# Optimization experiments

Measured on AMD Instinct MI355X. Metric: run time of the kernel, lower is better.

Reference implementation:

```python
import jax, jax.numpy as jnp
import numpy as np

N, E, D = 100000, 640000, 128  # nodes, edges, feature dim (in_dim == out_dim == 128)
BN_EPS = 1e-5


def setup_inputs() -> dict:
    key = jax.random.key(0)
    ks = jax.random.split(key, 8)
    x = jax.random.normal(ks[0], (N, D), dtype=jnp.float32)
    edge_index = jax.random.randint(ks[1], (2, E), 0, N, dtype=jnp.int64)
    s = 1.0 / np.sqrt(D)
    W1 = jax.random.uniform(ks[2], (D, D), jnp.float32, -s, s)
    b1 = jax.random.uniform(ks[3], (D,), jnp.float32, -s, s)
    W2 = jax.random.uniform(ks[4], (D, D), jnp.float32, -s, s)
    b2 = jax.random.uniform(ks[5], (D,), jnp.float32, -s, s)
    return {
        "x": x,
        "edge_index": edge_index,
        "eps": jnp.array([0.1], dtype=jnp.float32),
        "W1": W1, "b1": b1,
        "g1": jnp.ones((D,), jnp.float32), "beta1": jnp.zeros((D,), jnp.float32),
        "W2": W2, "b2": b2,
        "g2": jnp.ones((D,), jnp.float32), "beta2": jnp.zeros((D,), jnp.float32),
    }


def _batchnorm(h, gamma, beta):
    # BatchNorm1d in training mode: biased batch stats over the node dim
    mean = jnp.mean(h, axis=0)
    var = jnp.var(h, axis=0)
    return gamma * (h - mean) * jax.lax.rsqrt(var + BN_EPS) + beta


def reference(x, edge_index, eps, W1, b1, g1, beta1, W2, b2, g2, beta2):
    src, dst = edge_index[0], edge_index[1]
    # gather messages from source nodes, scatter-add into destination nodes
    aggr = jax.ops.segment_sum(x[src], dst, num_segments=x.shape[0])  # [N, D]
    h = (1.0 + eps) * x + aggr
    h = jax.nn.relu(_batchnorm(h @ W1.T + b1, g1, beta1))
    h = jax.nn.relu(_batchnorm(h @ W2.T + b2, g2, beta2))
    return h
```

## Files before the change

kernel.cpp:

```cpp
#include <hip/hip_runtime.h>

#define NN 100000
#define DD 128
#define EE 640000
#define NPAD 100352

typedef __bf16 bf16x8 __attribute__((ext_vector_type(8)));
typedef float floatx4 __attribute__((ext_vector_type(4)));

union BF8 {
    bf16x8 v;
    unsigned short u[8];
    int4 i4;
};

__device__ __forceinline__ unsigned short f2bf(float f) {
    unsigned int u = __float_as_uint(f);
    u += 0x7FFF + ((u >> 16) & 1);
    return (unsigned short)(u >> 16);
}

__global__ __launch_bounds__(256) void hist_k(const int* __restrict__ ei,
                                              int* __restrict__ deg) {
    int e = blockIdx.x * 256 + threadIdx.x;
    if (e < EE) atomicAdd(&deg[ei[EE + e]], 1);
}

__global__ __launch_bounds__(256) void scan1_k(const int* __restrict__ deg,
                                               int* __restrict__ exc,
                                               int* __restrict__ chunkSums) {
    __shared__ int s[256];
    int t = threadIdx.x, g = blockIdx.x * 256 + t;
    int v = (g < NN) ? deg[g] : 0;
    s[t] = v;
    __syncthreads();
    for (int off = 1; off < 256; off <<= 1) {
        int u = (t >= off) ? s[t - off] : 0;
        __syncthreads();
        s[t] += u;
        __syncthreads();
    }
    if (g < NN) exc[g] = s[t] - v;
    if (t == 255) chunkSums[blockIdx.x] = s[255];
}

__global__ __launch_bounds__(512) void scan2_k(int* __restrict__ chunkSums, int n) {
    __shared__ int s[512];
    int t = threadIdx.x;
    int v = (t < n) ? chunkSums[t] : 0;
    s[t] = v;
    __syncthreads();
    for (int off = 1; off < 512; off <<= 1) {
        int u = (t >= off) ? s[t - off] : 0;
        __syncthreads();
        s[t] += u;
        __syncthreads();
    }
    if (t < n) chunkSums[t] = s[t] - v;
}

__global__ __launch_bounds__(256) void scan3_k(int* __restrict__ exc,
                                               const int* __restrict__ chunkSums,
                                               int* __restrict__ cursor) {
    int g = blockIdx.x * 256 + threadIdx.x;
    if (g < NN) {
        int o = exc[g] + chunkSums[blockIdx.x];
        exc[g] = o;
        cursor[g] = o;
    }
}

__global__ __launch_bounds__(256) void esort_k(const int* __restrict__ ei,
                                               int* __restrict__ cursor,
                                               int* __restrict__ ssrc) {
    int e = blockIdx.x * 256 + threadIdx.x;
    if (e >= EE) return;
    int pos = atomicAdd(&cursor[ei[EE + e]], 1);
    ssrc[pos] = ei[e];
}

__global__ __launch_bounds__(256) void wconv_k(const float* __restrict__ W1,
                                               const float* __restrict__ W2,
                                               unsigned short* __restrict__ wb) {
    int i = blockIdx.x * 256 + threadIdx.x;
    const float4* s4 = (i < 4096) ? (const float4*)W1 : (const float4*)W2;
    float4 v = s4[i & 4095];
    ushort4 u;
    u.x = f2bf(v.x); u.y = f2bf(v.y); u.z = f2bf(v.z); u.w = f2bf(v.w);
    ((ushort4*)wb)[i] = u;
}

__global__ __launch_bounds__(256) void aggregate_k(
    const float4* __restrict__ x4, const int* __restrict__ ssrc,
    const int* __restrict__ offs, const int* __restrict__ deg,
    const float* __restrict__ epsp, ushort4* __restrict__ hout) {
    int tid = blockIdx.x * 256 + threadIdx.x;
    int node = tid >> 5, lane = tid & 31;
    if (node >= NN) return;
    int start = offs[node], d = deg[node];
    float ef = 1.0f + epsp[0];
    float4 v = x4[node * 32 + lane];
    float ax = ef * v.x, ay = ef * v.y, az = ef * v.z, aw = ef * v.w;
    for (int j = 0; j < d; j += 4) {
        int r = d - j;
        int b = start + j;
        int s0 = ssrc[b];
        int s1 = ssrc[b + ((r > 1) ? 1 : 0)];
        int s2 = ssrc[b + ((r > 2) ? 2 : 0)];
        int s3 = ssrc[b + ((r > 3) ? 3 : 0)];
        float4 xa = x4[s0 * 32 + lane];
        float4 xb = x4[s1 * 32 + lane];
        float4 xc = x4[s2 * 32 + lane];
        float4 xd = x4[s3 * 32 + lane];
        float m1 = (r > 1) ? 1.f : 0.f;
        float m2 = (r > 2) ? 1.f : 0.f;
        float m3 = (r > 3) ? 1.f : 0.f;
        ax += xa.x; ay += xa.y; az += xa.z; aw += xa.w;
        ax += m1 * xb.x; ay += m1 * xb.y; az += m1 * xb.z; aw += m1 * xb.w;
        ax += m2 * xc.x; ay += m2 * xc.y; az += m2 * xc.z; aw += m2 * xc.w;
        ax += m3 * xd.x; ay += m3 * xd.y; az += m3 * xd.z; aw += m3 * xd.w;
    }
    ushort4 u;
    u.x = f2bf(ax); u.y = f2bf(ay); u.z = f2bf(az); u.w = f2bf(aw);
    hout[node * 32 + lane] = u;
}

__global__ __launch_bounds__(256, 2) void gin_gemm_k(
    const unsigned short* __restrict__ hin,
    const unsigned short* __restrict__ Wbf, const float* __restrict__ bias,
    float* __restrict__ y, float* __restrict__ statsOut) {
    __shared__ __align__(16) float s_sum[128];
    __shared__ __align__(16) float s_sq[128];

    const int tid = threadIdx.x;
    const int l = tid & 63, w = tid >> 6;
    const int m = l & 15, q = l >> 4;

    if (tid < 128) { s_sum[tid] = 0.f; s_sq[tid] = 0.f; }

    bf16x8 wf[8][4];
#pragma unroll
    for (int ct = 0; ct < 8; ++ct) {
        const unsigned short* wr = Wbf + (size_t)(ct * 16 + m) * 128 + q * 8;
#pragma unroll
        for (int kc = 0; kc < 4; ++kc) {
            BF8 t;
            t.i4 = *(const int4*)(wr + kc * 32);
            wf[ct][kc] = t.v;
        }
    }
    float bc[8];
#pragma unroll
    for (int ct = 0; ct < 8; ++ct) bc[ct] = bias[ct * 16 + m];

    float ps[8], pq[8];
#pragma unroll
    for (int ct = 0; ct < 8; ++ct) { ps[ct] = 0.f; pq[ct] = 0.f; }

    __syncthreads();

    const int NT = NN / 16;
    const int stride = gridDim.x * 4;
    int t = blockIdx.x * 4 + w;

    const unsigned short* abase = hin + (size_t)m * 128 + q * 8;

    int4 ra[4];
    if (t < NT) {
        const unsigned short* ap = abase + (size_t)t * (16 * 128);
#pragma unroll
        for (int kc = 0; kc < 4; ++kc) ra[kc] = *(const int4*)(ap + kc * 32);
    }

    while (t < NT) {
        bf16x8 a[4];
#pragma unroll
        for (int kc = 0; kc < 4; ++kc) { BF8 tt; tt.i4 = ra[kc]; a[kc] = tt.v; }

        int tn = t + stride;
        if (tn < NT) {
            const unsigned short* ap = abase + (size_t)tn * (16 * 128);
#pragma unroll
            for (int kc = 0; kc < 4; ++kc) ra[kc] = *(const int4*)(ap + kc * 32);
        }

        floatx4 acc[8];
#pragma unroll
        for (int ct = 0; ct < 8; ++ct) acc[ct] = (floatx4)0.0f;
#pragma unroll
        for (int kc = 0; kc < 4; ++kc)
#pragma unroll
            for (int ct = 0; ct < 8; ++ct)
                acc[ct] = __builtin_amdgcn_mfma_f32_16x16x32_bf16(a[kc], wf[ct][kc], acc[ct], 0, 0, 0);

        float* yb = y + (size_t)(t * 16 + q * 4) * 128 + m;
#pragma unroll
        for (int ct = 0; ct < 8; ++ct) {
#pragma unroll
            for (int i = 0; i < 4; ++i) {
                float yv = acc[ct][i] + bc[ct];
                yb[(size_t)i * 128 + ct * 16] = yv;
                ps[ct] += yv;
                pq[ct] += yv * yv;
            }
        }
        t = tn;
    }

#pragma unroll
    for (int ct = 0; ct < 8; ++ct) {
        atomicAdd(&s_sum[ct * 16 + m], ps[ct]);
        atomicAdd(&s_sq[ct * 16 + m], pq[ct]);
    }
    __syncthreads();
    if (tid < 128) {
        unsafeAtomicAdd(&statsOut[tid], s_sum[tid]);
        unsafeAtomicAdd(&statsOut[128 + tid], s_sq[tid]);
    }
}

template <int OUT_BF16>
__global__ __launch_bounds__(256) void bn_relu_k(
    const float* __restrict__ y, const float* __restrict__ stats,
    const float* __restrict__ g, const float* __restrict__ beta,
    float* outf, unsigned short* __restrict__ outh) {
    __shared__ __align__(16) float sc[128];
    __shared__ __align__(16) float sh[128];
    int t = threadIdx.x;
    if (t < 128) {
        const float inv = 1.0f / (float)NN;
        float mean = stats[t] * inv;
        float var = stats[128 + t] * inv - mean * mean;
        float s = g[t] * rsqrtf(var + 1e-5f);
        sc[t] = s;
        sh[t] = beta[t] - mean * s;
    }
    __syncthreads();
    const int total4 = NN * 32;
    const float4* y4 = (const float4*)y;
    for (int i = blockIdx.x * 256 + t; i < total4; i += gridDim.x * 256) {
        int c4 = i & 31;
        float4 v = y4[i];
        float4 s = ((const float4*)sc)[c4];
        float4 b = ((const float4*)sh)[c4];
        float r0 = fmaxf(v.x * s.x + b.x, 0.f);
        float r1 = fmaxf(v.y * s.y + b.y, 0.f);
        float r2 = fmaxf(v.z * s.z + b.z, 0.f);
        float r3 = fmaxf(v.w * s.w + b.w, 0.f);
        if (OUT_BF16) {
            ushort4 u;
            u.x = f2bf(r0); u.y = f2bf(r1); u.z = f2bf(r2); u.w = f2bf(r3);
            ((ushort4*)outh)[i] = u;
        } else {
            ((float4*)outf)[i] = make_float4(r0, r1, r2, r3);
        }
    }
}

extern "C" void kernel_launch(void* const* d_in, const int* in_sizes, int n_in,
                              void* d_out, int out_size, void* d_ws, size_t ws_size,
                              hipStream_t stream) {
    const float* x   = (const float*)d_in[0];
    const int* ei    = (const int*)d_in[1];
    const float* eps = (const float*)d_in[2];
    const float* W1  = (const float*)d_in[3];
    const float* b1  = (const float*)d_in[4];
    const float* g1  = (const float*)d_in[5];
    const float* be1 = (const float*)d_in[6];
    const float* W2  = (const float*)d_in[7];
    const float* b2  = (const float*)d_in[8];
    const float* g2  = (const float*)d_in[9];
    const float* be2 = (const float*)d_in[10];
    float* out = (float*)d_out;

    int* deg        = (int*)d_ws;
    int* offs       = deg + NPAD;
    int* cursor     = offs + NPAD;
    int* chunkSums  = cursor + NPAD;
    int* ssrc       = chunkSums + 512;
    unsigned short* hbuf = (unsigned short*)(ssrc + EE + 256);
    float* stats    = (float*)(hbuf + (size_t)NN * DD);
    unsigned short* wbf = (unsigned short*)(stats + 512);

    hipMemsetAsync(deg, 0, NPAD * sizeof(int), stream);
    hipMemsetAsync(stats, 0, 512 * sizeof(float), stream);

    const int numChunks = (NN + 255) / 256;
    hist_k<<<(EE + 255) / 256, 256, 0, stream>>>(ei, deg);
    scan1_k<<<numChunks, 256, 0, stream>>>(deg, offs, chunkSums);
    scan2_k<<<1, 512, 0, stream>>>(chunkSums, numChunks);
    scan3_k<<<numChunks, 256, 0, stream>>>(offs, chunkSums, cursor);
    esort_k<<<(EE + 255) / 256, 256, 0, stream>>>(ei, cursor, ssrc);
    aggregate_k<<<(NN * 32 + 255) / 256, 256, 0, stream>>>(
        (const float4*)x, ssrc, offs, deg, eps, (ushort4*)hbuf);
    wconv_k<<<32, 256, 0, stream>>>(W1, W2, wbf);

    const int gblocks = 512;
    gin_gemm_k<<<gblocks, 256, 0, stream>>>(hbuf, wbf, b1, out, stats);
    bn_relu_k<1><<<4096, 256, 0, stream>>>(out, stats, g1, be1, nullptr, hbuf);
    gin_gemm_k<<<gblocks, 256, 0, stream>>>(hbuf, wbf + 16384, b2, out, stats + 256);
    bn_relu_k<0><<<4096, 256, 0, stream>>>(out, stats + 256, g2, be2, out, nullptr);
}
```

Before: 321.0 us.

## Fuse first BatchNorm+ReLU into second GEMM load and unroll aggregation by eight

The second GEMM now reads the fp32 output of the first GEMM directly. It applies the BN1 scale/shift and ReLU in registers and converts to bf16 on the fly, which removes the separate bn_relu pass and its bf16 intermediate buffer. The gather-aggregate loop now handles 8 neighbours per iteration instead of 4 and carries an occupancy hint, to keep more loads in flight. In exchange, the fused GEMM reads fp32 instead of bf16, doing twice the A-operand traffic, and it reads and writes the same buffer in place despite both pointers being marked restrict.

```diff
diff --git a/kernel.cpp b/kernel.cpp
--- a/kernel.cpp
+++ b/kernel.cpp
@@ -90,7 +90,7 @@
     ((ushort4*)wb)[i] = u;
 }
 
-__global__ __launch_bounds__(256) void aggregate_k(
+__global__ __launch_bounds__(256, 4) void aggregate_k(
     const float4* __restrict__ x4, const int* __restrict__ ssrc,
     const int* __restrict__ offs, const int* __restrict__ deg,
     const float* __restrict__ epsp, ushort4* __restrict__ hout) {
@@ -101,42 +101,76 @@
     float ef = 1.0f + epsp[0];
     float4 v = x4[node * 32 + lane];
     float ax = ef * v.x, ay = ef * v.y, az = ef * v.z, aw = ef * v.w;
-    for (int j = 0; j < d; j += 4) {
+    for (int j = 0; j < d; j += 8) {
         int r = d - j;
         int b = start + j;
         int s0 = ssrc[b];
         int s1 = ssrc[b + ((r > 1) ? 1 : 0)];
         int s2 = ssrc[b + ((r > 2) ? 2 : 0)];
         int s3 = ssrc[b + ((r > 3) ? 3 : 0)];
-        float4 xa = x4[s0 * 32 + lane];
-        float4 xb = x4[s1 * 32 + lane];
-        float4 xc = x4[s2 * 32 + lane];
-        float4 xd = x4[s3 * 32 + lane];
+        int s4i = ssrc[b + ((r > 4) ? 4 : 0)];
+        int s5 = ssrc[b + ((r > 5) ? 5 : 0)];
+        int s6 = ssrc[b + ((r > 6) ? 6 : 0)];
+        int s7 = ssrc[b + ((r > 7) ? 7 : 0)];
+        float4 x0 = x4[s0 * 32 + lane];
+        float4 x1 = x4[s1 * 32 + lane];
+        float4 x2 = x4[s2 * 32 + lane];
+        float4 x3 = x4[s3 * 32 + lane];
+        float4 x4v = x4[s4i * 32 + lane];
+        float4 x5 = x4[s5 * 32 + lane];
+        float4 x6 = x4[s6 * 32 + lane];
+        float4 x7 = x4[s7 * 32 + lane];
         float m1 = (r > 1) ? 1.f : 0.f;
         float m2 = (r > 2) ? 1.f : 0.f;
         float m3 = (r > 3) ? 1.f : 0.f;
-        ax += xa.x; ay += xa.y; az += xa.z; aw += xa.w;
-        ax += m1 * xb.x; ay += m1 * xb.y; az += m1 * xb.z; aw += m1 * xb.w;
-        ax += m2 * xc.x; ay += m2 * xc.y; az += m2 * xc.z; aw += m2 * xc.w;
-        ax += m3 * xd.x; ay += m3 * xd.y; az += m3 * xd.z; aw += m3 * xd.w;
+        float m4 = (r > 4) ? 1.f : 0.f;
+        float m5 = (r > 5) ? 1.f : 0.f;
+        float m6 = (r > 6) ? 1.f : 0.f;
+        float m7 = (r > 7) ? 1.f : 0.f;
+        ax += x0.x; ay += x0.y; az += x0.z; aw += x0.w;
+        ax += m1 * x1.x; ay += m1 * x1.y; az += m1 * x1.z; aw += m1 * x1.w;
+        ax += m2 * x2.x; ay += m2 * x2.y; az += m2 * x2.z; aw += m2 * x2.w;
+        ax += m3 * x3.x; ay += m3 * x3.y; az += m3 * x3.z; aw += m3 * x3.w;
+        ax += m4 * x4v.x; ay += m4 * x4v.y; az += m4 * x4v.z; aw += m4 * x4v.w;
+        ax += m5 * x5.x; ay += m5 * x5.y; az += m5 * x5.z; aw += m5 * x5.w;
+        ax += m6 * x6.x; ay += m6 * x6.y; az += m6 * x6.z; aw += m6 * x6.w;
+        ax += m7 * x7.x; ay += m7 * x7.y; az += m7 * x7.z; aw += m7 * x7.w;
     }
     ushort4 u;
     u.x = f2bf(ax); u.y = f2bf(ay); u.z = f2bf(az); u.w = f2bf(aw);
     hout[node * 32 + lane] = u;
 }
 
+template <int FUSE_BN>
 __global__ __launch_bounds__(256, 2) void gin_gemm_k(
     const unsigned short* __restrict__ hin,
+    const float* __restrict__ yin,
+    const float* __restrict__ statsIn,
+    const float* __restrict__ gmm,
+    const float* __restrict__ bta,
     const unsigned short* __restrict__ Wbf, const float* __restrict__ bias,
     float* __restrict__ y, float* __restrict__ statsOut) {
     __shared__ __align__(16) float s_sum[128];
     __shared__ __align__(16) float s_sq[128];
+    __shared__ __align__(16) float sc[128];
+    __shared__ __align__(16) float sh[128];
 
     const int tid = threadIdx.x;
     const int l = tid & 63, w = tid >> 6;
     const int m = l & 15, q = l >> 4;
 
-    if (tid < 128) { s_sum[tid] = 0.f; s_sq[tid] = 0.f; }
+    if (tid < 128) {
+        s_sum[tid] = 0.f;
+        s_sq[tid] = 0.f;
+        if (FUSE_BN) {
+            const float inv = 1.0f / (float)NN;
+            float mean = statsIn[tid] * inv;
+            float var = statsIn[128 + tid] * inv - mean * mean;
+            float s = gmm[tid] * rsqrtf(var + 1e-5f);
+            sc[tid] = s;
+            sh[tid] = bta[tid] - mean * s;
+        }
+    }
 
     bf16x8 wf[8][4];
 #pragma unroll
@@ -164,24 +198,62 @@
     int t = blockIdx.x * 4 + w;
 
     const unsigned short* abase = hin + (size_t)m * 128 + q * 8;
+    const float* ybase = yin + (size_t)m * 128 + q * 8;
 
     int4 ra[4];
+    float4 rf[8];
     if (t < NT) {
-        const unsigned short* ap = abase + (size_t)t * (16 * 128);
-#pragma unroll
-        for (int kc = 0; kc < 4; ++kc) ra[kc] = *(const int4*)(ap + kc * 32);
+        if (FUSE_BN) {
+            const float* yp = ybase + (size_t)t * (16 * 128);
+#pragma unroll
+            for (int i = 0; i < 8; ++i)
+                rf[i] = *(const float4*)(yp + (i >> 1) * 32 + (i & 1) * 4);
+        } else {
+            const unsigned short* ap = abase + (size_t)t * (16 * 128);
+#pragma unroll
+            for (int kc = 0; kc < 4; ++kc) ra[kc] = *(const int4*)(ap + kc * 32);
+        }
     }
 
     while (t < NT) {
         bf16x8 a[4];
 #pragma unroll
-        for (int kc = 0; kc < 4; ++kc) { BF8 tt; tt.i4 = ra[kc]; a[kc] = tt.v; }
+        for (int kc = 0; kc < 4; ++kc) {
+            if (FUSE_BN) {
+                float4 v0 = rf[2 * kc], v1 = rf[2 * kc + 1];
+                float4 s0 = *(const float4*)(sc + kc * 32 + q * 8);
+                float4 s1 = *(const float4*)(sc + kc * 32 + q * 8 + 4);
+                float4 h0 = *(const float4*)(sh + kc * 32 + q * 8);
+                float4 h1 = *(const float4*)(sh + kc * 32 + q * 8 + 4);
+                BF8 tt;
+                tt.u[0] = f2bf(fmaxf(v0.x * s0.x + h0.x, 0.f));
+                tt.u[1] = f2bf(fmaxf(v0.y * s0.y + h0.y, 0.f));
+                tt.u[2] = f2bf(fmaxf(v0.z * s0.z + h0.z, 0.f));
+                tt.u[3] = f2bf(fmaxf(v0.w * s0.w + h0.w, 0.f));
+                tt.u[4] = f2bf(fmaxf(v1.x * s1.x + h1.x, 0.f));
+                tt.u[5] = f2bf(fmaxf(v1.y * s1.y + h1.y, 0.f));
+                tt.u[6] = f2bf(fmaxf(v1.z * s1.z + h1.z, 0.f));
+                tt.u[7] = f2bf(fmaxf(v1.w * s1.w + h1.w, 0.f));
+                a[kc] = tt.v;
+            } else {
+                BF8 tt;
+                tt.i4 = ra[kc];
+                a[kc] = tt.v;
+            }
+        }
 
         int tn = t + stride;
         if (tn < NT) {
-            const unsigned short* ap = abase + (size_t)tn * (16 * 128);
-#pragma unroll
-            for (int kc = 0; kc < 4; ++kc) ra[kc] = *(const int4*)(ap + kc * 32);
+            if (FUSE_BN) {
+                const float* yp = ybase + (size_t)tn * (16 * 128);
+#pragma unroll
+                for (int i = 0; i < 8; ++i)
+                    rf[i] = *(const float4*)(yp + (i >> 1) * 32 + (i & 1) * 4);
+            } else {
+                const unsigned short* ap = abase + (size_t)tn * (16 * 128);
+#pragma unroll
+                for (int kc = 0; kc < 4; ++kc) ra[kc] = *(const int4*)(ap + kc * 32);
+            }
         }
 
         floatx4 acc[8];
@@ -219,11 +291,10 @@
     }
 }
 
-template <int OUT_BF16>
 __global__ __launch_bounds__(256) void bn_relu_k(
     const float* __restrict__ y, const float* __restrict__ stats,
     const float* __restrict__ g, const float* __restrict__ beta,
-    float* outf, unsigned short* __restrict__ outh) {
+    float* __restrict__ outf) {
     __shared__ __align__(16) float sc[128];
     __shared__ __align__(16) float sh[128];
     int t = threadIdx.x;
@@ -247,13 +318,7 @@
         float r1 = fmaxf(v.y * s.y + b.y, 0.f);
         float r2 = fmaxf(v.z * s.z + b.z, 0.f);
         float r3 = fmaxf(v.w * s.w + b.w, 0.f);
-        if (OUT_BF16) {
-            ushort4 u;
-            u.x = f2bf(r0); u.y = f2bf(r1); u.z = f2bf(r2); u.w = f2bf(r3);
-            ((ushort4*)outh)[i] = u;
-        } else {
-            ((float4*)outf)[i] = make_float4(r0, r1, r2, r3);
-        }
+        ((float4*)outf)[i] = make_float4(r0, r1, r2, r3);
     }
 }
 
@@ -296,8 +361,9 @@
     wconv_k<<<32, 256, 0, stream>>>(W1, W2, wbf);
 
     const int gblocks = 512;
-    gin_gemm_k<<<gblocks, 256, 0, stream>>>(hbuf, wbf, b1, out, stats);
-    bn_relu_k<1><<<4096, 256, 0, stream>>>(out, stats, g1, be1, nullptr, hbuf);
-    gin_gemm_k<<<gblocks, 256, 0, stream>>>(hbuf, wbf + 16384, b2, out, stats + 256);
-    bn_relu_k<0><<<4096, 256, 0, stream>>>(out, stats + 256, g2, be2, out, nullptr);
-}
+    gin_gemm_k<0><<<gblocks, 256, 0, stream>>>(
+        hbuf, nullptr, nullptr, nullptr, nullptr, wbf, b1, out, stats);
+    gin_gemm_k<1><<<gblocks, 256, 0, stream>>>(
+        nullptr, out, stats, g1, be1, wbf + 16384, b2, out, stats + 256);
+    bn_relu_k<<<4096, 256, 0, stream>>>(out, stats + 256, g2, be2, out);
+}
```

Result: slower. 336.1 us (+4.7%).
